# Kernel tuning notes

Measured on AMD Instinct MI355X. Metric: run time of the kernel, lower is better.

Reference implementation:

```python
import jax, jax.numpy as jnp
import numpy as np

BETA = 1.0  # cfg.TRAINING.beta
B, S, D = 128, 256, 1024


def setup_inputs() -> dict:
    key = jax.random.key(0)
    k1, k2, k3 = jax.random.split(key, 3)
    bridges = jax.random.normal(k1, (B, S, D), dtype=jnp.float32)
    # monotone increasing timestamps per row (true_divide-safe: bt>bp>bh)
    b_inx = jnp.arange(B * S, dtype=jnp.int32).reshape(B, S)
    # negative indices: one per positive position j in [1, S-2];
    # (idx + 1 + r) % dim guarantees neg_i != i and neg_j != j
    neg_i = (jnp.arange(B, dtype=jnp.int32)[:, None] + 1
             + jax.random.randint(k2, (B, S - 2), 0, B - 1, dtype=jnp.int32)) % B
    neg_j = (jnp.arange(1, S - 1, dtype=jnp.int32)[None, :] + 1
             + jax.random.randint(k3, (B, S - 2), 0, S - 1, dtype=jnp.int32)) % S
    return {"bridges": bridges, "b_inx": b_inx, "neg_i": neg_i, "neg_j": neg_j}


def reference(bridges, b_inx, neg_i, neg_j):
    dt = bridges.dtype
    t = b_inx.astype(dt)
    th = t[:, :1]            # [B,1] head timestamp
    tt = t[:, -1:]           # [B,1] tail timestamp
    tp = t[:, 1:-1]          # [B,S-2] positive timestamps
    alpha = (tp - th) / (tt - th)          # [B,S-2]
    sigma = alpha * (tt - tp)              # [B,S-2]

    head = bridges[:, 0]                   # [B,D]
    tail = bridges[:, -1]                  # [B,D]
    pos = bridges[:, 1:-1]                 # [B,S-2,D]
    neg = bridges[neg_i, neg_j]            # [B,S-2,D]

    a = alpha[..., None]
    mix = (1.0 - a) * head[:, None, :] + a * tail[:, None, :]  # [B,S-2,D]
    xp = pos - mix
    xn = neg - mix
    inv = 1.0 / (2.0 * sigma * sigma)
    pos_dis = -jnp.sum(xp * xp, axis=-1) * inv   # -||x||^2 / (2 sigma^2)
    neg_dis = -jnp.sum(xn * xn, axis=-1) * inv

    cur = pos_dis - neg_dis + jnp.asarray(BETA, dt)
    loss = jnp.sum(jnp.where(cur > 0, cur, jnp.zeros((), dt)))
    return loss / bridges.shape[0]
```

## Files before the change

kernel.cpp:

```cpp
#include <hip/hip_runtime.h>

constexpr int   Bc   = 128;
constexpr int   Sc   = 256;
constexpr int   Dc   = 1024;
constexpr float BETA = 1.0f;
constexpr int   NP   = Bc * (Sc - 2);
constexpr int   NR   = Bc * Sc;

constexpr size_t OFF_CNT  = 0;
constexpr size_t OFF_OFFS = 131072;
constexpr size_t OFF_SLOT = 262656;
constexpr size_t OFF_ROW  = 392704;
constexpr size_t OFF_LIST = 522752;
constexpr size_t OFF_POS  = 652800;
constexpr size_t OFF_NEG  = 782848;

__global__ __launch_bounds__(256) void k_build(
    const int* __restrict__ neg_i, const int* __restrict__ neg_j,
    int* __restrict__ cnt, int* __restrict__ slotv, int* __restrict__ rowid)
{
    int p = blockIdx.x * 256 + threadIdx.x;
    if (p >= NP) return;
    int r = neg_i[p] * Sc + neg_j[p];
    rowid[p] = r;
    slotv[p] = atomicAdd(&cnt[r], 1);
}

__global__ __launch_bounds__(1024) void k_scan(
    const int* __restrict__ cnt, int* __restrict__ offs)
{
    __shared__ int part[1024];
    const int t = threadIdx.x;
    const int base = t * 32;
    int s = 0;
#pragma unroll
    for (int i = 0; i < 32; ++i) s += cnt[base + i];
    part[t] = s;
    __syncthreads();
    for (int d = 1; d < 1024; d <<= 1) {
        int v = (t >= d) ? part[t - d] : 0;
        __syncthreads();
        part[t] += v;
        __syncthreads();
    }
    int run = (t == 0) ? 0 : part[t - 1];
#pragma unroll
    for (int i = 0; i < 32; ++i) {
        offs[base + i] = run;
        run += cnt[base + i];
    }
    if (t == 1023) offs[NR] = run;
}

__global__ __launch_bounds__(256) void k_scatter(
    const int* __restrict__ offs, const int* __restrict__ slotv,
    const int* __restrict__ rowid, int* __restrict__ list)
{
    int p = blockIdx.x * 256 + threadIdx.x;
    if (p >= NP) return;
    int b = p / (Sc - 2);
    int j = p - b * (Sc - 2);
    list[offs[rowid[p]] + slotv[p]] = (b << 8) | j;
}

__global__ __launch_bounds__(256) void k_main(
    const float* __restrict__ bridges, const int* __restrict__ b_inx,
    const int* __restrict__ offs, const int* __restrict__ list,
    float* __restrict__ pos_dis, float* __restrict__ neg_dis)
{
    const int wid  = (blockIdx.x * 256 + threadIdx.x) >> 6;
    const int lane = threadIdx.x & 63;
    const int r    = wid;
    const int b    = r >> 8;
    const int s    = r & 255;

    const float4* __restrict__ row4 = (const float4*)bridges;

    float4 x[4];
    {
        const float4* rp = row4 + (size_t)r * (Dc / 4);
#pragma unroll
        for (int k = 0; k < 4; ++k) x[k] = rp[k * 64 + lane];
    }

    const int beg = offs[r], end = offs[r + 1];

    if (s >= 1 && s <= Sc - 2) {
        const float th = (float)b_inx[b * Sc];
        const float tt = (float)b_inx[b * Sc + (Sc - 1)];
        const float tp = (float)b_inx[b * Sc + s];
        const float alpha = (tp - th) / (tt - th);
        const float sigma = alpha * (tt - tp);
        const float inv   = 1.0f / (2.0f * sigma * sigma);
        const float4* hp = row4 + (size_t)(b * Sc) * (Dc / 4);
        const float4* tq = row4 + (size_t)(b * Sc + Sc - 1) * (Dc / 4);
        float d = 0.0f;
#pragma unroll
        for (int k = 0; k < 4; ++k) {
            const float4 h = hp[k * 64 + lane];
            const float4 t = tq[k * 64 + lane];
            const float m0 = fmaf(alpha, t.x - h.x, h.x);
            const float m1 = fmaf(alpha, t.y - h.y, h.y);
            const float m2 = fmaf(alpha, t.z - h.z, h.z);
            const float m3 = fmaf(alpha, t.w - h.w, h.w);
            const float e0 = x[k].x - m0, e1 = x[k].y - m1;
            const float e2 = x[k].z - m2, e3 = x[k].w - m3;
            d += e0 * e0 + e1 * e1 + e2 * e2 + e3 * e3;
        }
#pragma unroll
        for (int m = 32; m >= 1; m >>= 1) d += __shfl_xor(d, m);
        if (lane == 0) pos_dis[b * (Sc - 2) + (s - 1)] = -d * inv;
    }

    for (int q = beg; q < end; ++q) {
        const int e  = list[q];
        const int bb = e >> 8;
        const int jj = e & 255;
        const int ss = jj + 1;
        const float th = (float)b_inx[bb * Sc];
        const float tt = (float)b_inx[bb * Sc + (Sc - 1)];
        const float tp = (float)b_inx[bb * Sc + ss];
        const float alpha = (tp - th) / (tt - th);
        const float sigma = alpha * (tt - tp);
        const float inv   = 1.0f / (2.0f * sigma * sigma);
        const float4* hp = row4 + (size_t)(bb * Sc) * (Dc / 4);
        const float4* tq = row4 + (size_t)(bb * Sc + Sc - 1) * (Dc / 4);
        float d = 0.0f;
#pragma unroll
        for (int k = 0; k < 4; ++k) {
            const float4 h = hp[k * 64 + lane];
            const float4 t = tq[k * 64 + lane];
            const float m0 = fmaf(alpha, t.x - h.x, h.x);
            const float m1 = fmaf(alpha, t.y - h.y, h.y);
            const float m2 = fmaf(alpha, t.z - h.z, h.z);
            const float m3 = fmaf(alpha, t.w - h.w, h.w);
            const float e0 = x[k].x - m0, e1 = x[k].y - m1;
            const float e2 = x[k].z - m2, e3 = x[k].w - m3;
            d += e0 * e0 + e1 * e1 + e2 * e2 + e3 * e3;
        }
#pragma unroll
        for (int m = 32; m >= 1; m >>= 1) d += __shfl_xor(d, m);
        if (lane == 0) neg_dis[bb * (Sc - 2) + jj] = -d * inv;
    }
}

__global__ __launch_bounds__(1024) void k_reduce(
    const float* __restrict__ pos_dis, const float* __restrict__ neg_dis,
    float* __restrict__ out)
{
    __shared__ float red[1024];
    const int t = threadIdx.x;
    float a = 0.0f;
    for (int p = t; p < NP; p += 1024) {
        const float cur = pos_dis[p] - neg_dis[p] + BETA;
        if (cur > 0.0f) a += cur;
    }
    red[t] = a;
    __syncthreads();
    for (int d = 512; d > 0; d >>= 1) {
        if (t < d) red[t] += red[t + d];
        __syncthreads();
    }
    if (t == 0) out[0] = red[0] * (1.0f / (float)Bc);
}

extern "C" void kernel_launch(void* const* d_in, const int* in_sizes, int n_in,
                              void* d_out, int out_size, void* d_ws, size_t ws_size,
                              hipStream_t stream) {
    const float* bridges = (const float*)d_in[0];
    const int*   b_inx   = (const int*)d_in[1];
    const int*   neg_i   = (const int*)d_in[2];
    const int*   neg_j   = (const int*)d_in[3];
    float*       out     = (float*)d_out;

    char* ws = (char*)d_ws;
    int*   cnt     = (int*)(ws + OFF_CNT);
    int*   offs    = (int*)(ws + OFF_OFFS);
    int*   slotv   = (int*)(ws + OFF_SLOT);
    int*   rowid   = (int*)(ws + OFF_ROW);
    int*   list    = (int*)(ws + OFF_LIST);
    float* pos_dis = (float*)(ws + OFF_POS);
    float* neg_dis = (float*)(ws + OFF_NEG);

    hipMemsetAsync(cnt, 0, NR * sizeof(int), stream);
    k_build  <<<(NP + 255) / 256, 256, 0, stream>>>(neg_i, neg_j, cnt, slotv, rowid);
    k_scan   <<<1, 1024, 0, stream>>>(cnt, offs);
    k_scatter<<<(NP + 255) / 256, 256, 0, stream>>>(offs, slotv, rowid, list);
    k_main   <<<NR / 4, 256, 0, stream>>>(bridges, b_inx, offs, list, pos_dis, neg_dis);
    k_reduce <<<1, 1024, 0, stream>>>(pos_dis, neg_dis, out);
}
```

Before: 227.6 us.

## Replace count-scan-scatter bucketing with fixed-capacity buckets plus overflow list

Drops the single-block prefix scan and the scatter kernel by giving each target row a fixed-capacity slot array filled directly in the build kernel via atomics. Entries beyond the capacity go to a global overflow list, which the final single-block reduce kernel processes before summing. This removes two kernel launches and a serial scan, at the cost of a larger workspace and a possibly slow single-block overflow path if collisions are heavy. NP/256 is exact, so the bounds check is removed.

Result: faster. 217.9 us (-4.3%).

```diff
diff --git a/kernel.cpp b/kernel.cpp
--- a/kernel.cpp
+++ b/kernel.cpp
@@ -6,71 +6,39 @@
 constexpr float BETA = 1.0f;
 constexpr int   NP   = Bc * (Sc - 2);
 constexpr int   NR   = Bc * Sc;
+constexpr int   CAP  = 32;
 
 constexpr size_t OFF_CNT  = 0;
-constexpr size_t OFF_OFFS = 131072;
-constexpr size_t OFF_SLOT = 262656;
-constexpr size_t OFF_ROW  = 392704;
-constexpr size_t OFF_LIST = 522752;
-constexpr size_t OFF_POS  = 652800;
-constexpr size_t OFF_NEG  = 782848;
+constexpr size_t OFF_OVFC = 131072;
+constexpr size_t OFF_LIST = 131200;
+constexpr size_t OFF_OVFL = OFF_LIST + (size_t)NR * CAP * 4;
+constexpr size_t OFF_POS  = OFF_OVFL + (size_t)NP * 4;
+constexpr size_t OFF_NEG  = OFF_POS  + (size_t)NP * 4;
 
 __global__ __launch_bounds__(256) void k_build(
     const int* __restrict__ neg_i, const int* __restrict__ neg_j,
-    int* __restrict__ cnt, int* __restrict__ slotv, int* __restrict__ rowid)
+    int* __restrict__ cnt, int* __restrict__ list,
+    int* __restrict__ ovf_cnt, int* __restrict__ ovf_list)
 {
-    int p = blockIdx.x * 256 + threadIdx.x;
-    if (p >= NP) return;
-    int r = neg_i[p] * Sc + neg_j[p];
-    rowid[p] = r;
-    slotv[p] = atomicAdd(&cnt[r], 1);
-}
-
-__global__ __launch_bounds__(1024) void k_scan(
-    const int* __restrict__ cnt, int* __restrict__ offs)
-{
-    __shared__ int part[1024];
-    const int t = threadIdx.x;
-    const int base = t * 32;
-    int s = 0;
-#pragma unroll
-    for (int i = 0; i < 32; ++i) s += cnt[base + i];
-    part[t] = s;
-    __syncthreads();
-    for (int d = 1; d < 1024; d <<= 1) {
-        int v = (t >= d) ? part[t - d] : 0;
-        __syncthreads();
-        part[t] += v;
-        __syncthreads();
-    }
-    int run = (t == 0) ? 0 : part[t - 1];
-#pragma unroll
-    for (int i = 0; i < 32; ++i) {
-        offs[base + i] = run;
-        run += cnt[base + i];
-    }
-    if (t == 1023) offs[NR] = run;
-}
-
-__global__ __launch_bounds__(256) void k_scatter(
-    const int* __restrict__ offs, const int* __restrict__ slotv,
-    const int* __restrict__ rowid, int* __restrict__ list)
-{
-    int p = blockIdx.x * 256 + threadIdx.x;
-    if (p >= NP) return;
-    int b = p / (Sc - 2);
-    int j = p - b * (Sc - 2);
-    list[offs[rowid[p]] + slotv[p]] = (b << 8) | j;
+    const int p = blockIdx.x * 256 + threadIdx.x;
+    const int b = p / (Sc - 2);
+    const int j = p - b * (Sc - 2);
+    const int r = neg_i[p] * Sc + neg_j[p];
+    const int slot = atomicAdd(&cnt[r], 1);
+    if (slot < CAP) {
+        list[r * CAP + slot] = (b << 8) | j;
+    } else {
+        ovf_list[atomicAdd(ovf_cnt, 1)] = p;
+    }
 }
 
 __global__ __launch_bounds__(256) void k_main(
     const float* __restrict__ bridges, const int* __restrict__ b_inx,
-    const int* __restrict__ offs, const int* __restrict__ list,
+    const int* __restrict__ cnt, const int* __restrict__ list,
     float* __restrict__ pos_dis, float* __restrict__ neg_dis)
 {
-    const int wid  = (blockIdx.x * 256 + threadIdx.x) >> 6;
+    const int r    = (blockIdx.x * 256 + threadIdx.x) >> 6;
     const int lane = threadIdx.x & 63;
-    const int r    = wid;
     const int b    = r >> 8;
     const int s    = r & 255;
 
@@ -83,7 +51,7 @@
         for (int k = 0; k < 4; ++k) x[k] = rp[k * 64 + lane];
     }
 
-    const int beg = offs[r], end = offs[r + 1];
+    const int nneg = min(cnt[r], CAP);
 
     if (s >= 1 && s <= Sc - 2) {
         const float th = (float)b_inx[b * Sc];
@@ -112,8 +80,8 @@
         if (lane == 0) pos_dis[b * (Sc - 2) + (s - 1)] = -d * inv;
     }
 
-    for (int q = beg; q < end; ++q) {
-        const int e  = list[q];
+    for (int q = 0; q < nneg; ++q) {
+        const int e  = list[r * CAP + q];
         const int bb = e >> 8;
         const int jj = e & 255;
         const int ss = jj + 1;
@@ -145,11 +113,54 @@
 }
 
 __global__ __launch_bounds__(1024) void k_reduce(
-    const float* __restrict__ pos_dis, const float* __restrict__ neg_dis,
+    const float* __restrict__ bridges, const int* __restrict__ b_inx,
+    const int* __restrict__ neg_i, const int* __restrict__ neg_j,
+    const int* __restrict__ ovf_cnt, const int* __restrict__ ovf_list,
+    const float* __restrict__ pos_dis, float* __restrict__ neg_dis,
     float* __restrict__ out)
 {
+    const int t    = threadIdx.x;
+    const int wave = t >> 6;
+    const int lane = t & 63;
+    const float4* __restrict__ row4 = (const float4*)bridges;
+
+    const int novf = *ovf_cnt;
+    for (int e = wave; e < novf; e += 16) {
+        const int p  = ovf_list[e];
+        const int bb = p / (Sc - 2);
+        const int jj = p - bb * (Sc - 2);
+        const int ss = jj + 1;
+        const int r  = neg_i[p] * Sc + neg_j[p];
+        const float th = (float)b_inx[bb * Sc];
+        const float tt = (float)b_inx[bb * Sc + (Sc - 1)];
+        const float tp = (float)b_inx[bb * Sc + ss];
+        const float alpha = (tp - th) / (tt - th);
+        const float sigma = alpha * (tt - tp);
+        const float inv   = 1.0f / (2.0f * sigma * sigma);
+        const float4* xp = row4 + (size_t)r * (Dc / 4);
+        const float4* hp = row4 + (size_t)(bb * Sc) * (Dc / 4);
+        const float4* tq = row4 + (size_t)(bb * Sc + Sc - 1) * (Dc / 4);
+        float d = 0.0f;
+#pragma unroll
+        for (int k = 0; k < 4; ++k) {
+            const float4 x = xp[k * 64 + lane];
+            const float4 h = hp[k * 64 + lane];
+            const float4 tv = tq[k * 64 + lane];
+            const float m0 = fmaf(alpha, tv.x - h.x, h.x);
+            const float m1 = fmaf(alpha, tv.y - h.y, h.y);
+            const float m2 = fmaf(alpha, tv.z - h.z, h.z);
+            const float m3 = fmaf(alpha, tv.w - h.w, h.w);
+            const float e0 = x.x - m0, e1 = x.y - m1;
+            const float e2 = x.z - m2, e3 = x.w - m3;
+            d += e0 * e0 + e1 * e1 + e2 * e2 + e3 * e3;
+        }
+#pragma unroll
+        for (int m = 32; m >= 1; m >>= 1) d += __shfl_xor(d, m);
+        if (lane == 0) neg_dis[bb * (Sc - 2) + jj] = -d * inv;
+    }
+    __syncthreads();
+
     __shared__ float red[1024];
-    const int t = threadIdx.x;
     float a = 0.0f;
     for (int p = t; p < NP; p += 1024) {
         const float cur = pos_dis[p] - neg_dis[p] + BETA;
@@ -174,18 +185,16 @@
     float*       out     = (float*)d_out;
 
     char* ws = (char*)d_ws;
-    int*   cnt     = (int*)(ws + OFF_CNT);
-    int*   offs    = (int*)(ws + OFF_OFFS);
-    int*   slotv   = (int*)(ws + OFF_SLOT);
-    int*   rowid   = (int*)(ws + OFF_ROW);
-    int*   list    = (int*)(ws + OFF_LIST);
-    float* pos_dis = (float*)(ws + OFF_POS);
-    float* neg_dis = (float*)(ws + OFF_NEG);
-
-    hipMemsetAsync(cnt, 0, NR * sizeof(int), stream);
-    k_build  <<<(NP + 255) / 256, 256, 0, stream>>>(neg_i, neg_j, cnt, slotv, rowid);
-    k_scan   <<<1, 1024, 0, stream>>>(cnt, offs);
-    k_scatter<<<(NP + 255) / 256, 256, 0, stream>>>(offs, slotv, rowid, list);
-    k_main   <<<NR / 4, 256, 0, stream>>>(bridges, b_inx, offs, list, pos_dis, neg_dis);
-    k_reduce <<<1, 1024, 0, stream>>>(pos_dis, neg_dis, out);
-}
+    int*   cnt      = (int*)(ws + OFF_CNT);
+    int*   ovf_cnt  = (int*)(ws + OFF_OVFC);
+    int*   list     = (int*)(ws + OFF_LIST);
+    int*   ovf_list = (int*)(ws + OFF_OVFL);
+    float* pos_dis  = (float*)(ws + OFF_POS);
+    float* neg_dis  = (float*)(ws + OFF_NEG);
+
+    hipMemsetAsync(ws, 0, OFF_OVFC + 4, stream);
+    k_build <<<NP / 256, 256, 0, stream>>>(neg_i, neg_j, cnt, list, ovf_cnt, ovf_list);
+    k_main  <<<NR / 4, 256, 0, stream>>>(bridges, b_inx, cnt, list, pos_dis, neg_dis);
+    k_reduce<<<1, 1024, 0, stream>>>(bridges, b_inx, neg_i, neg_j,
+                                     ovf_cnt, ovf_list, pos_dis, neg_dis, out);
+}
```
